# Optimization experiments

Measured on AMD Instinct MI355X. Metric: run time of the kernel, lower is better.

## Reference

```python
import jax, jax.numpy as jnp
import numpy as np

ALPHA = 0.2   # LeakyReLU negative slope
RATIO = 0.5   # blend ratio between attention and structural similarity
KHOP = 3      # k-hop structural similarity depth
NEG_BIG = -9e15


def _build_adj(edge, n):
    # edge: [N, D] int neighbor indices; adj[i, edge[i, d]] = 1
    rows = jnp.broadcast_to(jnp.arange(n)[:, None], edge.shape)
    return jnp.zeros((n, n), jnp.float32).at[rows, edge].set(1.0)


def _structural_similarity(adj, khop):
    # Sum of adjacency powers A + A^2 + ... + A^khop (k-hop reachability counts).
    s = adj
    p = adj
    for _ in range(khop - 1):
        p = p @ adj
        s = s + p
    return s


def _per_graph(atom, edge, W, a):
    n = atom.shape[0]
    adj = _build_adj(edge, n)
    structure = jax.nn.softmax(_structural_similarity(adj, KHOP), axis=1)
    h = atom @ W                                   # [N, F]
    f = h.shape[1]
    # a_input[i,j] = concat(h_i, h_j); a_input @ a == (h @ a1)_i + (h @ a2)_j
    src = h @ a[:f, 0]                             # [N]
    dst = h @ a[f:, 0]                             # [N]
    e = jax.nn.leaky_relu(src[:, None] + dst[None, :], ALPHA)  # [N, N]
    att = jnp.where(adj > 0, e, NEG_BIG)
    att = jax.nn.softmax(att, axis=1)
    blended = RATIO * att + (1.0 - RATIO) * structure
    return jax.nn.elu(blended @ h)                 # [N, F]


def setup_inputs() -> dict:
    key = jax.random.key(0)
    k1, k2, k3, k4 = jax.random.split(key, 4)
    B, N, D, F_IN, F_OUT = 16, 1024, 8, 128, 64
    atoms = jax.random.normal(k1, (B, N, F_IN), dtype=jnp.float32)
    edges = jax.random.randint(k2, (B, N, D), 0, N, dtype=jnp.int64)
    W = jax.random.normal(k3, (F_IN, F_OUT), dtype=jnp.float32) * 0.1
    a = jax.random.normal(k4, (2 * F_OUT, 1), dtype=jnp.float32) * 0.1
    return {"atoms": atoms, "edges": edges, "W": W, "a": a}


def reference(atoms, edges, W, a):
    return jax.vmap(_per_graph, in_axes=(0, 0, None, None))(atoms, edges, W, a)
```

## Files before the change

kernel.cpp:

```cpp
#include <hip/hip_runtime.h>

#define NN 1024
#define DG 8
#define FO 64
#define FI 128
#define LALPHA 0.2f
#define BR 16
#define SBS 257
#define RDS 68

typedef __attribute__((ext_vector_type(8))) short bf16x8;
typedef __attribute__((ext_vector_type(4))) float f32x4;

static __device__ __forceinline__ unsigned short f2bf(float x) {
  union { float f; unsigned u; } v; v.f = x;
  unsigned r = v.u + 0x7FFFu + ((v.u >> 16) & 1u);
  return (unsigned short)(r >> 16);
}
static __device__ __forceinline__ float bf2f(unsigned short h) {
  union { unsigned u; float f; } v; v.u = ((unsigned)h) << 16;
  return v.f;
}

__global__ __launch_bounds__(256) void k_prep(const float* __restrict__ atoms,
                                              const float* __restrict__ W,
                                              const float* __restrict__ a,
                                              const int* __restrict__ edges,
                                              int* __restrict__ uniq,
                                              ushort* __restrict__ hT,
                                              ushort* __restrict__ hN,
                                              float* __restrict__ srcv,
                                              float* __restrict__ dstv) {
  __shared__ float sp[16], dp[16];
  const int t = threadIdx.x, b = blockIdx.x;
  const int g = b >> 6;
  const int rbase = b * 16;

  if (t < 16) {
    sp[t] = 0.f; dp[t] = 0.f;
    const int rr = rbase + t;
    int e[DG];
#pragma unroll
    for (int s = 0; s < DG; s++) e[s] = edges[rr * DG + s];
#pragma unroll
    for (int s = 0; s < DG; s++) {
      int v = e[s];
      bool dup = false;
#pragma unroll
      for (int q = 0; q < DG; q++)
        if (q < s && e[q] == v) dup = true;
      uniq[rr * DG + s] = dup ? -1 : v;
    }
  }

  const int w = t >> 6, lane = t & 63, quad = lane >> 4, l16 = lane & 15;
  const float* __restrict__ Ar = atoms + (size_t)(rbase + l16) * FI;
  const float* __restrict__ Wc = W + w * 16 + l16;
  f32x4 acc = {0.f, 0.f, 0.f, 0.f};
#pragma unroll
  for (int kc = 0; kc < 4; kc++) {
    const int k0 = kc * 32 + quad * 8;
    float4 a0 = *(const float4*)(Ar + k0);
    float4 a1 = *(const float4*)(Ar + k0 + 4);
    float av[8] = {a0.x, a0.y, a0.z, a0.w, a1.x, a1.y, a1.z, a1.w};
    float wv[8];
#pragma unroll
    for (int e = 0; e < 8; e++) wv[e] = Wc[(k0 + e) * FO];
    bf16x8 ahi, alo, bhi, blo;
#pragma unroll
    for (int e = 0; e < 8; e++) {
      ushort h = f2bf(av[e]);
      ahi[e] = (short)h;
      alo[e] = (short)f2bf(av[e] - bf2f(h));
      ushort g2 = f2bf(wv[e]);
      bhi[e] = (short)g2;
      blo[e] = (short)f2bf(wv[e] - bf2f(g2));
    }
    acc = __builtin_amdgcn_mfma_f32_16x16x32_bf16(ahi, bhi, acc, 0, 0, 0);
    acc = __builtin_amdgcn_mfma_f32_16x16x32_bf16(ahi, blo, acc, 0, 0, 0);
    acc = __builtin_amdgcn_mfma_f32_16x16x32_bf16(alo, bhi, acc, 0, 0, 0);
  }

  const int f = w * 16 + l16;
  const float as_ = a[f], ad_ = a[FO + f];
  float ps[4], pd[4];
#pragma unroll
  for (int r = 0; r < 4; r++) {
    float v = acc[r];
    int rb = rbase + quad * 4 + r;
    ushort hv = f2bf(v);
    hT[((size_t)g * FO + f) * NN + (rb & (NN - 1))] = hv;
    hN[(size_t)rb * FO + f] = hv;
    ps[r] = v * as_;
    pd[r] = v * ad_;
  }
#pragma unroll
  for (int off = 1; off < 16; off <<= 1)
#pragma unroll
    for (int r = 0; r < 4; r++) {
      ps[r] += __shfl_xor(ps[r], off);
      pd[r] += __shfl_xor(pd[r], off);
    }
  __syncthreads();
  if (l16 == 0) {
#pragma unroll
    for (int r = 0; r < 4; r++) {
      atomicAdd(&sp[quad * 4 + r], ps[r]);
      atomicAdd(&dp[quad * 4 + r], pd[r]);
    }
  }
  __syncthreads();
  if (t < 16) {
    srcv[rbase + t] = sp[t];
    dstv[rbase + t] = dp[t];
  }
}

__global__ __launch_bounds__(256, 4) void k_fused(const int* __restrict__ uniq,
                                                  const float* __restrict__ srcv,
                                                  const float* __restrict__ dstv,
                                                  const ushort* __restrict__ hT,
                                                  const ushort* __restrict__ hN,
                                                  float* __restrict__ out) {
  __shared__ unsigned Sb[BR * SBS];
  __shared__ __align__(16) float red[4][BR][RDS];
  __shared__ float zred[4][16];
  __shared__ int n1[BR][DG];
  __shared__ float attw[BR][DG];
  __shared__ float lutF[80];
  __shared__ ushort lutB[80];

  const int t = threadIdx.x, b = blockIdx.x;
  const int g = b >> 6, rbase = (b & 63) * BR;
  const int* __restrict__ Ug = uniq + (size_t)g * NN * DG;

  for (int i = t; i < BR * SBS; i += 256) Sb[i] = 0u;
  if (t < BR * DG) n1[t >> 3][t & 7] = Ug[(rbase + (t >> 3)) * DG + (t & 7)];
  if (t >= 128 && t < 208) {
    int c = t - 128;
    float e = __expf((float)c);
    lutF[c] = e;
    lutB[c] = f2bf(e);
  }
  __syncthreads();

#pragma unroll
  for (int q = 0; q < 4; q++) {
    int idx = t + 256 * q;
    int r = idx & 15, e = idx >> 4;
    int j = n1[r][e >> 3];
    if (j >= 0) {
      if ((e & 7) == 0)
        atomicAdd(&Sb[r * SBS + (j >> 2)], 1u << ((j & 3) * 8));
      int k = Ug[j * DG + (e & 7)];
      if (k >= 0) {
        atomicAdd(&Sb[r * SBS + (k >> 2)], 1u << ((k & 3) * 8));
        int4 m0 = *(const int4*)(Ug + k * DG);
        int4 m1 = *(const int4*)(Ug + k * DG + 4);
        int ll[8] = {m0.x, m0.y, m0.z, m0.w, m1.x, m1.y, m1.z, m1.w};
#pragma unroll
        for (int e2 = 0; e2 < 8; e2++)
          if (ll[e2] >= 0) atomicAdd(&Sb[r * SBS + (ll[e2] >> 2)], 1u << ((ll[e2] & 3) * 8));
      }
    }
  }
  if (t < BR) {
    int r = t;
    float si = srcv[g * NN + rbase + r];
    float ev[DG];
    float m = -1e30f;
#pragma unroll
    for (int s = 0; s < DG; s++) {
      int j = n1[r][s];
      if (j >= 0) {
        float x = si + dstv[g * NN + j];
        x = x > 0.f ? x : LALPHA * x;
        ev[s] = x;
        m = fmaxf(m, x);
      } else ev[s] = -1e30f;
    }
    float sm = 0.f;
#pragma unroll
    for (int s = 0; s < DG; s++) {
      float e = (n1[r][s] >= 0) ? __expf(ev[s] - m) : 0.f;
      ev[s] = e;
      sm += e;
    }
    float inv = 1.f / sm;
#pragma unroll
    for (int s = 0; s < DG; s++) attw[r][s] = ev[s] * inv;
  }
  __syncthreads();

  const int rr_ = t >> 4, f0_ = (t & 15) * 4;
  float ah0 = 0.f, ah1 = 0.f, ah2 = 0.f, ah3 = 0.f;
#pragma unroll
  for (int s = 0; s < DG; s++) {
    int j = n1[rr_][s];
    if (j >= 0) {
      float wgt = attw[rr_][s];
      uint2 hv = *(const uint2*)(hN + ((size_t)(g * NN + j)) * FO + f0_);
      ah0 += wgt * bf2f((ushort)(hv.x & 0xffffu));
      ah1 += wgt * bf2f((ushort)(hv.x >> 16));
      ah2 += wgt * bf2f((ushort)(hv.y & 0xffffu));
      ah3 += wgt * bf2f((ushort)(hv.y >> 16));
    }
  }

  const int v = t >> 6, lane = t & 63, quad = lane >> 4, l16 = lane & 15;
  const int k0 = v * 256;
  const ushort* __restrict__ hb = hT + ((size_t)g * FO) * NN;
  f32x4 acc[4] = {{0.f, 0.f, 0.f, 0.f}, {0.f, 0.f, 0.f, 0.f},
                  {0.f, 0.f, 0.f, 0.f}, {0.f, 0.f, 0.f, 0.f}};
  float zacc = 0.f;
#pragma unroll
  for (int ks = 0; ks < 256; ks += 32) {
    const int wd = l16 * SBS + ((k0 + ks) >> 2) + quad * 2;
    unsigned s0 = Sb[wd], s1 = Sb[wd + 1];
    const int c0 = s0 & 255u, c1 = (s0 >> 8) & 255u, c2 = (s0 >> 16) & 255u, c3 = s0 >> 24;
    const int c4 = s1 & 255u, c5 = (s1 >> 8) & 255u, c6 = (s1 >> 16) & 255u, c7 = s1 >> 24;
    bf16x8 af;
    af[0] = (short)lutB[c0]; af[1] = (short)lutB[c1];
    af[2] = (short)lutB[c2]; af[3] = (short)lutB[c3];
    af[4] = (short)lutB[c4]; af[5] = (short)lutB[c5];
    af[6] = (short)lutB[c6]; af[7] = (short)lutB[c7];
    zacc += (lutF[c0] + lutF[c1]) + (lutF[c2] + lutF[c3]) +
            (lutF[c4] + lutF[c5]) + (lutF[c6] + lutF[c7]);
    const ushort* hp = hb + (size_t)l16 * NN + k0 + ks + quad * 8;
#pragma unroll
    for (int ct = 0; ct < 4; ct++) {
      bf16x8 bf = *(const bf16x8*)(hp + (size_t)(ct * 16) * NN);
      acc[ct] = __builtin_amdgcn_mfma_f32_16x16x32_bf16(af, bf, acc[ct], 0, 0, 0);
    }
  }
  zacc += __shfl_xor(zacc, 16);
  zacc += __shfl_xor(zacc, 32);
  if (lane < 16) zred[v][lane] = zacc;
#pragma unroll
  for (int ct = 0; ct < 4; ct++)
#pragma unroll
    for (int r = 0; r < 4; r++)
      red[v][quad * 4 + r][ct * 16 + l16] = acc[ct][r];
  __syncthreads();

  const float Z = zred[0][rr_] + zred[1][rr_] + zred[2][rr_] + zred[3][rr_];
  const float hz = 0.5f / Z;
  f32x4 s = *(const f32x4*)&red[0][rr_][f0_];
  f32x4 s1v = *(const f32x4*)&red[1][rr_][f0_];
  f32x4 s2v = *(const f32x4*)&red[2][rr_][f0_];
  f32x4 s3v = *(const f32x4*)&red[3][rr_][f0_];
  float o0 = 0.5f * ah0 + (s[0] + s1v[0] + s2v[0] + s3v[0]) * hz;
  float o1 = 0.5f * ah1 + (s[1] + s1v[1] + s2v[1] + s3v[1]) * hz;
  float o2 = 0.5f * ah2 + (s[2] + s1v[2] + s2v[2] + s3v[2]) * hz;
  float o3 = 0.5f * ah3 + (s[3] + s1v[3] + s2v[3] + s3v[3]) * hz;
  o0 = o0 > 0.f ? o0 : __expf(o0) - 1.f;
  o1 = o1 > 0.f ? o1 : __expf(o1) - 1.f;
  o2 = o2 > 0.f ? o2 : __expf(o2) - 1.f;
  o3 = o3 > 0.f ? o3 : __expf(o3) - 1.f;
  *(float4*)(out + ((size_t)(g * NN + rbase + rr_)) * FO + f0_) =
      make_float4(o0, o1, o2, o3);
}

extern "C" void kernel_launch(void* const* d_in, const int* in_sizes, int n_in,
                              void* d_out, int out_size, void* d_ws, size_t ws_size,
                              hipStream_t stream) {
  const float* atoms = (const float*)d_in[0];
  const int* edges = (const int*)d_in[1];
  const float* W = (const float*)d_in[2];
  const float* a = (const float*)d_in[3];
  float* out = (float*)d_out;

  const int nrows = in_sizes[0] / FI;
  const int ngraph = nrows / NN;

  ushort* hT = (ushort*)d_ws;
  ushort* hN = hT + (size_t)ngraph * FO * NN;
  float* srcv = (float*)(hN + (size_t)nrows * FO);
  float* dstv = srcv + nrows;
  int* uniq = (int*)(dstv + nrows);

  k_prep<<<nrows / 16, 256, 0, stream>>>(atoms, W, a, edges, uniq, hT, hN, srcv, dstv);
  k_fused<<<ngraph * (NN / BR), 256, 0, stream>>>(uniq, srcv, dstv, hT, hN, out);
}
```

Baseline: 97.62 us.

## Precompute per-node 2-hop count matrix and build k-hop rows by summing

Adds a kernel that materialises, for each node, its byte-packed 2-hop reachability counts (A^2 row) into a global N×N byte matrix per graph. The fused kernel then forms each row of A + A^2 + A^3 by loading the node's own A^2 row plus the A^2 rows of its neighbours and adding the direct-neighbour bits, replacing the scattered shared-memory atomics that walked all three hops. This trades shared atomics and dependent gathers for coalesced vector loads, but it adds an extra launch and a 16 MB write/read of byte counts to workspace. Byte-packed counts could overflow if many paths converge, the same risk as before.

After: 114.8 us. 1.18x slower.

```diff
diff --git a/kernel.cpp b/kernel.cpp
--- a/kernel.cpp
+++ b/kernel.cpp
@@ -116,11 +116,45 @@
   }
 }
 
+__global__ __launch_bounds__(256) void k_B(const int* __restrict__ uniq,
+                                           unsigned char* __restrict__ Bm) {
+  __shared__ unsigned Brow[64 * 256];
+  const int t = threadIdx.x, b = blockIdx.x;
+  const int g = b >> 4, jb = (b & 15) * 64;
+  const int* __restrict__ Ug = uniq + (size_t)g * NN * DG;
+
+  for (int i = t; i < 64 * 256; i += 256) Brow[i] = 0u;
+  __syncthreads();
+
+  const int jl = t >> 2, q = t & 3;
+  const int j = jb + jl;
+  int2 ss = *(const int2*)(Ug + j * DG + q * 2);
+#pragma unroll
+  for (int h = 0; h < 2; h++) {
+    int s = (h == 0) ? ss.x : ss.y;
+    if (s >= 0) {
+      int4 m0 = *(const int4*)(Ug + s * DG);
+      int4 m1 = *(const int4*)(Ug + s * DG + 4);
+      int ll[8] = {m0.x, m0.y, m0.z, m0.w, m1.x, m1.y, m1.z, m1.w};
+#pragma unroll
+      for (int e = 0; e < 8; e++)
+        if (ll[e] >= 0)
+          atomicAdd(&Brow[jl * 256 + (ll[e] >> 2)], 1u << ((ll[e] & 3) * 8));
+    }
+  }
+  __syncthreads();
+
+  uint4* dst = (uint4*)(Bm + ((size_t)g * NN + jb) * NN);
+  const uint4* src = (const uint4*)Brow;
+  for (int i = t; i < 64 * 64; i += 256) dst[i] = src[i];
+}
+
 __global__ __launch_bounds__(256, 4) void k_fused(const int* __restrict__ uniq,
                                                   const float* __restrict__ srcv,
                                                   const float* __restrict__ dstv,
                                                   const ushort* __restrict__ hT,
                                                   const ushort* __restrict__ hN,
+                                                  const unsigned char* __restrict__ Bm,
                                                   float* __restrict__ out) {
   __shared__ unsigned Sb[BR * SBS];
   __shared__ __align__(16) float red[4][BR][RDS];
@@ -133,8 +167,8 @@
   const int t = threadIdx.x, b = blockIdx.x;
   const int g = b >> 6, rbase = (b & 63) * BR;
   const int* __restrict__ Ug = uniq + (size_t)g * NN * DG;
-
-  for (int i = t; i < BR * SBS; i += 256) Sb[i] = 0u;
+  const unsigned char* __restrict__ Bg = Bm + (size_t)g * NN * NN;
+
   if (t < BR * DG) n1[t >> 3][t & 7] = Ug[(rbase + (t >> 3)) * DG + (t & 7)];
   if (t >= 128 && t < 208) {
     int c = t - 128;
@@ -144,25 +178,40 @@
   }
   __syncthreads();
 
-#pragma unroll
-  for (int q = 0; q < 4; q++) {
-    int idx = t + 256 * q;
-    int r = idx & 15, e = idx >> 4;
-    int j = n1[r][e >> 3];
-    if (j >= 0) {
-      if ((e & 7) == 0)
-        atomicAdd(&Sb[r * SBS + (j >> 2)], 1u << ((j & 3) * 8));
-      int k = Ug[j * DG + (e & 7)];
-      if (k >= 0) {
-        atomicAdd(&Sb[r * SBS + (k >> 2)], 1u << ((k & 3) * 8));
-        int4 m0 = *(const int4*)(Ug + k * DG);
-        int4 m1 = *(const int4*)(Ug + k * DG + 4);
-        int ll[8] = {m0.x, m0.y, m0.z, m0.w, m1.x, m1.y, m1.z, m1.w};
-#pragma unroll
-        for (int e2 = 0; e2 < 8; e2++)
-          if (ll[e2] >= 0) atomicAdd(&Sb[r * SBS + (ll[e2] >> 2)], 1u << ((ll[e2] & 3) * 8));
+  {
+    const int r = t >> 4, w16 = t & 15;
+    unsigned accw[16];
+    {
+      const uint4* bp = (const uint4*)(Bg + (size_t)(rbase + r) * NN + w16 * 64);
+      uint4 v0 = bp[0], v1 = bp[1], v2 = bp[2], v3 = bp[3];
+      accw[0] = v0.x; accw[1] = v0.y; accw[2] = v0.z; accw[3] = v0.w;
+      accw[4] = v1.x; accw[5] = v1.y; accw[6] = v1.z; accw[7] = v1.w;
+      accw[8] = v2.x; accw[9] = v2.y; accw[10] = v2.z; accw[11] = v2.w;
+      accw[12] = v3.x; accw[13] = v3.y; accw[14] = v3.z; accw[15] = v3.w;
+    }
+#pragma unroll
+    for (int s = 0; s < DG; s++) {
+      int j = n1[r][s];
+      if (j >= 0) {
+        const uint4* bp = (const uint4*)(Bg + (size_t)j * NN + w16 * 64);
+        uint4 v0 = bp[0], v1 = bp[1], v2 = bp[2], v3 = bp[3];
+        accw[0] += v0.x; accw[1] += v0.y; accw[2] += v0.z; accw[3] += v0.w;
+        accw[4] += v1.x; accw[5] += v1.y; accw[6] += v1.z; accw[7] += v1.w;
+        accw[8] += v2.x; accw[9] += v2.y; accw[10] += v2.z; accw[11] += v2.w;
+        accw[12] += v3.x; accw[13] += v3.y; accw[14] += v3.z; accw[15] += v3.w;
+        int rel = j - w16 * 64;
+        if (rel >= 0 && rel < 64) {
+          unsigned addv = 1u << ((rel & 3) * 8);
+          int wsel = rel >> 2;
+#pragma unroll
+          for (int i = 0; i < 16; i++)
+            if (wsel == i) accw[i] += addv;
+        }
       }
     }
+    unsigned* sbr = &Sb[r * SBS + w16 * 16];
+#pragma unroll
+    for (int i = 0; i < 16; i++) sbr[i] = accw[i];
   }
   if (t < BR) {
     int r = t;
@@ -278,7 +327,9 @@
   float* srcv = (float*)(hN + (size_t)nrows * FO);
   float* dstv = srcv + nrows;
   int* uniq = (int*)(dstv + nrows);
+  unsigned char* Bm = (unsigned char*)(uniq + (size_t)nrows * DG);
 
   k_prep<<<nrows / 16, 256, 0, stream>>>(atoms, W, a, edges, uniq, hT, hN, srcv, dstv);
-  k_fused<<<ngraph * (NN / BR), 256, 0, stream>>>(uniq, srcv, dstv, hT, hN, out);
-}
+  k_B<<<ngraph * (NN / 64), 256, 0, stream>>>(uniq, Bm);
+  k_fused<<<ngraph * (NN / BR), 256, 0, stream>>>(uniq, srcv, dstv, hT, hN, Bm, out);
+}
```
